# Kernel tuning notes

Hardware: AMD Instinct MI355X
Metric: run time of the kernel (lower is better)

## Reference

```python
import jax, jax.numpy as jnp
import numpy as np


def _cubic_coeffs(t):
    # Catmull-Rom-style weights used by the original bicubic_interpolate
    t2 = t * t
    t3 = t2 * t
    cm1 = (-t3 + 2.0 * t2 - t) / 2.0
    c0 = (3.0 * t3 - 5.0 * t2 + 2.0) / 2.0
    c1 = (-3.0 * t3 + 4.0 * t2 + t) / 2.0
    c2 = 1.0 - (cm1 + c0 + c1)
    return (cm1, c0, c1, c2)


def _warp_bicubic(input_image, delta_x, delta_y):
    B, C, H, W = input_image.shape
    BXC = B * C
    # identity meshgrid, normalized to [-1, 1] then mapped back (faithful to source)
    gx = jnp.arange(W, dtype=jnp.float32)[None, None, :]   # [1,1,W]
    gy = jnp.arange(H, dtype=jnp.float32)[None, :, None]   # [1,H,1]
    new_x = 2.0 * (gx + delta_x) / max(W - 1, 1) - 1.0     # [B,H,W]
    new_y = 2.0 * (gy + delta_y) / max(H - 1, 1) - 1.0
    # un-normalize to pixel coords; tile across channels exactly like X.repeat([C,1,1,1])
    x_map = jnp.tile((new_x + 1.0) * (W - 1) / 2.0, (C, 1, 1))  # [BXC,H,W]
    y_map = jnp.tile((new_y + 1.0) * (H - 1) / 2.0, (C, 1, 1))
    x0f = jnp.floor(x_map)
    y0f = jnp.floor(y_map)
    tx = x_map - x0f
    ty = y_map - y0f
    cx = _cubic_coeffs(tx)
    cy = _cubic_coeffs(ty)
    x0 = x0f.astype(jnp.int32)
    y0 = y0f.astype(jnp.int32)
    xs = [jnp.clip(x0 + o, 0, W - 1) for o in (-1, 0, 1, 2)]
    ys = [jnp.clip(y0 + o, 0, H - 1) for o in (-1, 0, 1, 2)]
    flat = input_image.reshape(-1)                          # b-major, c-minor
    base = (jnp.arange(BXC, dtype=jnp.int32) * (H * W))[:, None, None]
    out = jnp.zeros((BXC, H, W), dtype=jnp.float32)
    for i in range(4):
        row = jnp.zeros((BXC, H, W), dtype=jnp.float32)
        off_y = base + ys[i] * W
        for j in range(4):
            row = row + cx[j] * jnp.take(flat, off_y + xs[j])  # 16-tap gather
        out = out + cy[i] * row
    return out.reshape(B, C, H, W)


def setup_inputs() -> dict:
    key = jax.random.key(0)
    k1, k2, k3 = jax.random.split(key, 3)
    B, C, H, W = 8, 3, 1024, 1024
    return {
        "input_image": jax.random.normal(k1, (B, C, H, W), dtype=jnp.float32),
        "delta_x": jax.random.normal(k2, (B, H, W), dtype=jnp.float32),
        "delta_y": jax.random.normal(k3, (B, H, W), dtype=jnp.float32),
    }


def reference(input_image, delta_x, delta_y):
    # Warp_Object.forward with flag_bicubic_or_bilinear='bicubic',
    # delta maps shared across channels (3D delta branch).
    return _warp_bicubic(input_image, delta_x, delta_y)
```

## Files before the change

kernel.cpp:

```cpp
#include <hip/hip_runtime.h>
#include <hip/hip_fp16.h>


#define RT   6
#define ROWS 16
#define COLS 77
#define NPOS (ROWS * COLS)

struct alignas(8) Cell {
    __half2 a;
    __half2 b;
};

__device__ __forceinline__ void cubic_coeffs(float t, float c[4]) {
    float t2 = t * t;
    float t3 = t2 * t;
    c[0] = (-t3 + 2.0f * t2 - t) * 0.5f;
    c[1] = (3.0f * t3 - 5.0f * t2 + 2.0f) * 0.5f;
    c[2] = (-3.0f * t3 + 4.0f * t2 + t) * 0.5f;
    c[3] = 1.0f - (c[0] + c[1] + c[2]);
}

__global__ __launch_bounds__(256) void warp_bicubic_kernel(
    const float* __restrict__ img,
    const float* __restrict__ dx,
    const float* __restrict__ dy,
    float* __restrict__ out,
    int B, int C, int H, int W)
{
    __shared__ Cell lds[NPOS];

    const int tx = threadIdx.x;
    const int ty = threadIdx.y;
    const int tid = ty * 64 + tx;
    const int X = blockIdx.x * 64;
    const int Y = blockIdx.y * 4;
    const int db = blockIdx.z;
    const int hw = H * W;

    const float* __restrict__ ch0 = img + (size_t)db * hw;
    const float* __restrict__ ch1 = img + (size_t)(db + B) * hw;
    const float* __restrict__ ch2 = img + (size_t)(db + 2 * B) * hw;

    const bool interior = (X >= RT) && (X - RT + COLS <= W) &&
                          (Y >= RT) && (Y - RT + ROWS <= H);
    if (interior) {
        const float* __restrict__ b0 = ch0 + (size_t)(Y - RT) * W + (X - RT);
        const float* __restrict__ b1 = ch1 + (size_t)(Y - RT) * W + (X - RT);
        const float* __restrict__ b2 = ch2 + (size_t)(Y - RT) * W + (X - RT);
        int r = tid / COLS;
        int c = tid - r * COLS;
        int off = r * W + c;
        for (int p = tid; p < NPOS; p += 256) {
            Cell cell;
            cell.a = __floats2half2_rn(b0[off], b1[off]);
            cell.b = __floats2half2_rn(b2[off], 0.0f);
            lds[p] = cell;
            off += 3 * W + (256 - 3 * COLS);
            c += 256 - 3 * COLS;
            if (c >= COLS) { c -= COLS; off += W - COLS; }
        }
    } else {
        int r = tid / COLS;
        int c = tid - r * COLS;
        for (int p = tid; p < NPOS; p += 256) {
            int gy = min(max(Y - RT + r, 0), H - 1);
            int gx = min(max(X - RT + c, 0), W - 1);
            size_t off = (size_t)gy * W + gx;
            Cell cell;
            cell.a = __floats2half2_rn(ch0[off], ch1[off]);
            cell.b = __floats2half2_rn(ch2[off], 0.0f);
            lds[p] = cell;
            r += 3; c += 256 - 3 * COLS;
            if (c >= COLS) { c -= COLS; r += 1; }
        }
    }
    __syncthreads();

    const int x = X + tx;
    const int y = Y + ty;
    const int pos  = y * W + x;
    const int dofs = db * hw + pos;
    const float fdx = dx[dofs];
    const float fdy = dy[dofs];

    const float xm = (float)x + fdx;
    const float ym = (float)y + fdy;
    const float x0f = floorf(xm);
    const float y0f = floorf(ym);
    const float tfx = xm - x0f;
    const float tfy = ym - y0f;

    float cx[4], cy[4];
    cubic_coeffs(tfx, cx);
    cubic_coeffs(tfy, cy);

    const int x0 = (int)x0f;
    const int y0 = (int)y0f;

    float a0, a1, a2;

    const unsigned ulx = (unsigned)(x0 - X + (RT - 1));
    const unsigned uly = (unsigned)(y0 - Y + (RT - 1));

    if (ulx <= (unsigned)(COLS - 4) && uly <= (unsigned)(ROWS - 4)) {
        const Cell* __restrict__ base = lds + uly * COLS + ulx;
        __half2 acc01 = __float2half2_rn(0.0f);
        __half2 acc2  = __float2half2_rn(0.0f);
#pragma unroll
        for (int i = 0; i < 4; ++i) {
#pragma unroll
            for (int j = 0; j < 4; ++j) {
                Cell t = base[i * COLS + j];
                float wij = cy[i] * cx[j];
                __half2 w2 = __float2half2_rn(wij);
                acc01 = __hfma2(w2, t.a, acc01);
                acc2  = __hfma2(w2, t.b, acc2);
            }
        }
        a0 = __low2float(acc01);
        a1 = __high2float(acc01);
        a2 = __low2float(acc2);
    } else {
        a0 = a1 = a2 = 0.0f;
        int xs[4], rowoff[4];
#pragma unroll
        for (int o = 0; o < 4; ++o) {
            xs[o] = min(max(x0 - 1 + o, 0), W - 1);
            rowoff[o] = min(max(y0 - 1 + o, 0), H - 1) * W;
        }
#pragma unroll
        for (int i = 0; i < 4; ++i) {
            float w0 = cy[i] * cx[0], w1 = cy[i] * cx[1];
            float w2 = cy[i] * cx[2], w3 = cy[i] * cx[3];
            const float* r0 = ch0 + rowoff[i];
            const float* r1 = ch1 + rowoff[i];
            const float* r2 = ch2 + rowoff[i];
            a0 = fmaf(w0, r0[xs[0]], a0); a0 = fmaf(w1, r0[xs[1]], a0);
            a0 = fmaf(w2, r0[xs[2]], a0); a0 = fmaf(w3, r0[xs[3]], a0);
            a1 = fmaf(w0, r1[xs[0]], a1); a1 = fmaf(w1, r1[xs[1]], a1);
            a1 = fmaf(w2, r1[xs[2]], a1); a1 = fmaf(w3, r1[xs[3]], a1);
            a2 = fmaf(w0, r2[xs[0]], a2); a2 = fmaf(w1, r2[xs[1]], a2);
            a2 = fmaf(w2, r2[xs[2]], a2); a2 = fmaf(w3, r2[xs[3]], a2);
        }
    }

    out[(size_t)db * hw + pos] = a0;
    out[(size_t)(db + B) * hw + pos] = a1;
    out[(size_t)(db + 2 * B) * hw + pos] = a2;
}

extern "C" void kernel_launch(void* const* d_in, const int* in_sizes, int n_in,
                              void* d_out, int out_size, void* d_ws, size_t ws_size,
                              hipStream_t stream) {
    const float* img = (const float*)d_in[0];
    const float* dx  = (const float*)d_in[1];
    const float* dy  = (const float*)d_in[2];
    float* out = (float*)d_out;

    const int B = 8, C = 3, H = 1024, W = 1024;
    dim3 block(64, 4, 1);
    dim3 grid(W / 64, H / 4, B);
    warp_bicubic_kernel<<<grid, block, 0, stream>>>(img, dx, dy, out, B, C, H, W);
}
```

Measured before the change: 72.72 us.

## Enlarge block tile to 64x16 with float4 halo loads and separable fp16 filter

Block size grows from 64x4 to 64x16 threads, and the shared halo tile grows to 30x80 with a padded stride, so the halo overhead per output pixel shrinks. The tile is now loaded with float4 vector reads and 16-byte LDS stores instead of scalar loops. The 16-tap filter is split into separate row and column passes in fp16, which cuts the per-tap weight products and conversions. In exchange, more intermediate rounding in half precision can hurt accuracy, and 1024-thread blocks with a launch-bounds of 8 may pressure registers and occupancy.

```diff
diff --git a/kernel.cpp b/kernel.cpp
--- a/kernel.cpp
+++ b/kernel.cpp
@@ -2,15 +2,18 @@
 #include <hip/hip_fp16.h>
 
 
-#define RT   6
-#define ROWS 16
-#define COLS 77
-#define NPOS (ROWS * COLS)
+#define RTY 7
+#define RWS 30
+#define RTX 8
+#define CLS 80
+#define STR 82
+#define NQ  (RWS * (CLS / 4))
 
 struct alignas(8) Cell {
     __half2 a;
     __half2 b;
 };
+struct alignas(16) Cell2 { Cell c0, c1; };
 
 __device__ __forceinline__ void cubic_coeffs(float t, float c[4]) {
     float t2 = t * t;
@@ -21,20 +24,20 @@
     c[3] = 1.0f - (c[0] + c[1] + c[2]);
 }
 
-__global__ __launch_bounds__(256) void warp_bicubic_kernel(
+__global__ __launch_bounds__(1024, 8) void warp_bicubic_kernel(
     const float* __restrict__ img,
     const float* __restrict__ dx,
     const float* __restrict__ dy,
     float* __restrict__ out,
     int B, int C, int H, int W)
 {
-    __shared__ Cell lds[NPOS];
+    __shared__ Cell lds[RWS * STR];
 
     const int tx = threadIdx.x;
     const int ty = threadIdx.y;
     const int tid = ty * 64 + tx;
     const int X = blockIdx.x * 64;
-    const int Y = blockIdx.y * 4;
+    const int Y = blockIdx.y * 16;
     const int db = blockIdx.z;
     const int hw = H * W;
 
@@ -42,38 +45,38 @@
     const float* __restrict__ ch1 = img + (size_t)(db + B) * hw;
     const float* __restrict__ ch2 = img + (size_t)(db + 2 * B) * hw;
 
-    const bool interior = (X >= RT) && (X - RT + COLS <= W) &&
-                          (Y >= RT) && (Y - RT + ROWS <= H);
-    if (interior) {
-        const float* __restrict__ b0 = ch0 + (size_t)(Y - RT) * W + (X - RT);
-        const float* __restrict__ b1 = ch1 + (size_t)(Y - RT) * W + (X - RT);
-        const float* __restrict__ b2 = ch2 + (size_t)(Y - RT) * W + (X - RT);
-        int r = tid / COLS;
-        int c = tid - r * COLS;
-        int off = r * W + c;
-        for (int p = tid; p < NPOS; p += 256) {
-            Cell cell;
-            cell.a = __floats2half2_rn(b0[off], b1[off]);
-            cell.b = __floats2half2_rn(b2[off], 0.0f);
-            lds[p] = cell;
-            off += 3 * W + (256 - 3 * COLS);
-            c += 256 - 3 * COLS;
-            if (c >= COLS) { c -= COLS; off += W - COLS; }
+    if (tid < NQ) {
+        int r  = tid / 20;
+        int qc = tid - r * 20;
+        int gy  = Y - RTY + r;
+        int gx0 = X - RTX + 4 * qc;
+        Cell cells[4];
+        if (gy >= 0 && gy < H && gx0 >= 0 && gx0 <= W - 4) {
+            size_t off = (size_t)gy * W + gx0;
+            float4 v0 = *(const float4*)(ch0 + off);
+            float4 v1 = *(const float4*)(ch1 + off);
+            float4 v2 = *(const float4*)(ch2 + off);
+            cells[0].a = __floats2half2_rn(v0.x, v1.x);
+            cells[0].b = __floats2half2_rn(v2.x, 0.0f);
+            cells[1].a = __floats2half2_rn(v0.y, v1.y);
+            cells[1].b = __floats2half2_rn(v2.y, 0.0f);
+            cells[2].a = __floats2half2_rn(v0.z, v1.z);
+            cells[2].b = __floats2half2_rn(v2.z, 0.0f);
+            cells[3].a = __floats2half2_rn(v0.w, v1.w);
+            cells[3].b = __floats2half2_rn(v2.w, 0.0f);
+        } else {
+            int gyc = min(max(gy, 0), H - 1);
+#pragma unroll
+            for (int e = 0; e < 4; ++e) {
+                int gxc = min(max(gx0 + e, 0), W - 1);
+                size_t off = (size_t)gyc * W + gxc;
+                cells[e].a = __floats2half2_rn(ch0[off], ch1[off]);
+                cells[e].b = __floats2half2_rn(ch2[off], 0.0f);
+            }
         }
-    } else {
-        int r = tid / COLS;
-        int c = tid - r * COLS;
-        for (int p = tid; p < NPOS; p += 256) {
-            int gy = min(max(Y - RT + r, 0), H - 1);
-            int gx = min(max(X - RT + c, 0), W - 1);
-            size_t off = (size_t)gy * W + gx;
-            Cell cell;
-            cell.a = __floats2half2_rn(ch0[off], ch1[off]);
-            cell.b = __floats2half2_rn(ch2[off], 0.0f);
-            lds[p] = cell;
-            r += 3; c += 256 - 3 * COLS;
-            if (c >= COLS) { c -= COLS; r += 1; }
-        }
+        Cell2* dst = (Cell2*)&lds[r * STR + 4 * qc];
+        dst[0] = *(const Cell2*)&cells[0];
+        dst[1] = *(const Cell2*)&cells[2];
     }
     __syncthreads();
 
@@ -100,23 +103,36 @@
 
     float a0, a1, a2;
 
-    const unsigned ulx = (unsigned)(x0 - X + (RT - 1));
-    const unsigned uly = (unsigned)(y0 - Y + (RT - 1));
+    const unsigned ulx = (unsigned)(x0 - X + (RTX - 1));
+    const unsigned uly = (unsigned)(y0 - Y + (RTY - 1));
 
-    if (ulx <= (unsigned)(COLS - 4) && uly <= (unsigned)(ROWS - 4)) {
-        const Cell* __restrict__ base = lds + uly * COLS + ulx;
+    if (ulx <= (unsigned)(CLS - 4) && uly <= (unsigned)(RWS - 4)) {
+        const Cell* __restrict__ base = lds + uly * STR + ulx;
+        __half2 cxh[4], cyh[4];
+#pragma unroll
+        for (int j = 0; j < 4; ++j) {
+            cxh[j] = __float2half2_rn(cx[j]);
+            cyh[j] = __float2half2_rn(cy[j]);
+        }
         __half2 acc01 = __float2half2_rn(0.0f);
         __half2 acc2  = __float2half2_rn(0.0f);
 #pragma unroll
         for (int i = 0; i < 4; ++i) {
-#pragma unroll
-            for (int j = 0; j < 4; ++j) {
-                Cell t = base[i * COLS + j];
-                float wij = cy[i] * cx[j];
-                __half2 w2 = __float2half2_rn(wij);
-                acc01 = __hfma2(w2, t.a, acc01);
-                acc2  = __hfma2(w2, t.b, acc2);
-            }
+            const Cell* __restrict__ row = base + i * STR;
+            Cell t0 = row[0];
+            Cell t1 = row[1];
+            Cell t2 = row[2];
+            Cell t3 = row[3];
+            __half2 r01 = __hmul2(cxh[0], t0.a);
+            r01 = __hfma2(cxh[1], t1.a, r01);
+            r01 = __hfma2(cxh[2], t2.a, r01);
+            r01 = __hfma2(cxh[3], t3.a, r01);
+            __half2 r2 = __hmul2(cxh[0], t0.b);
+            r2 = __hfma2(cxh[1], t1.b, r2);
+            r2 = __hfma2(cxh[2], t2.b, r2);
+            r2 = __hfma2(cxh[3], t3.b, r2);
+            acc01 = __hfma2(cyh[i], r01, acc01);
+            acc2  = __hfma2(cyh[i], r2, acc2);
         }
         a0 = __low2float(acc01);
         a1 = __high2float(acc01);
@@ -159,7 +175,7 @@
     float* out = (float*)d_out;
 
     const int B = 8, C = 3, H = 1024, W = 1024;
-    dim3 block(64, 4, 1);
-    dim3 grid(W / 64, H / 4, B);
+    dim3 block(64, 16, 1);
+    dim3 grid(W / 64, H / 16, B);
     warp_bicubic_kernel<<<grid, block, 0, stream>>>(img, dx, dy, out, B, C, H, W);
 }
```

New measurement: 68.31 us. -6.1%, faster.
